# Kernel optimization log

Hardware: AMD Instinct MI355X
Metric: run time of the kernel (lower is better)

Reference implementation:

```python
import jax, jax.numpy as jnp
import numpy as np

ALPHA, GAMMA, EPS, BIG = 0.25, 2.0, 1e-7, 1e7
STRIDES = (8, 16, 32, 64, 128)
SHRINK = 0.2


def _project(boxes, fw, fh, stride):
    # shrink box around its center by SHRINK, project to feature grid (floor/ceil), clip
    cx = (boxes[..., 0] + boxes[..., 2]) * 0.5
    cy = (boxes[..., 1] + boxes[..., 3]) * 0.5
    hw = (boxes[..., 2] - boxes[..., 0]) * 0.5 * SHRINK
    hh = (boxes[..., 3] - boxes[..., 1]) * 0.5 * SHRINK
    x1 = jnp.clip(jnp.floor((cx - hw) / stride).astype(jnp.int32), 0, fw - 1)
    y1 = jnp.clip(jnp.floor((cy - hh) / stride).astype(jnp.int32), 0, fh - 1)
    x2 = jnp.clip(jnp.ceil((cx + hw) / stride).astype(jnp.int32), 1, fw)
    y2 = jnp.clip(jnp.ceil((cy + hh) / stride).astype(jnp.int32), 1, fh)
    return x1, y1, x2, y2


def _level_loss(cls_l, regr_l, boxes, labels, stride, fh, fw):
    # cls_l [B,fh,fw,C], regr_l [B,fh,fw,4], boxes [B,G,4], labels [B,G] -> loss [B,G]
    B, G = labels.shape
    x1, y1, x2, y2 = _project(boxes, fw, fh, stride)
    xs = jnp.arange(fw, dtype=jnp.int32)
    ys = jnp.arange(fh, dtype=jnp.int32)
    mx = (xs[None, None] >= x1[..., None]) & (xs[None, None] < x2[..., None])  # [B,G,fw]
    my = (ys[None, None] >= y1[..., None]) & (ys[None, None] < y2[..., None])  # [B,G,fh]
    mask = my[..., :, None] & mx[..., None, :]                                 # [B,G,fh,fw]
    denom = jnp.maximum(jnp.sum(mask, axis=(2, 3)).astype(cls_l.dtype), 1.0)   # = #positives

    # focal over one-hot(gt_label): sum_c = f0 - neg[gt] + pos[gt]
    p = jnp.clip(cls_l, EPS, 1.0 - EPS)
    neg = (1.0 - ALPHA) * p ** GAMMA * (-jnp.log1p(-p))   # per-class label=0 term
    pos = ALPHA * (1.0 - p) ** GAMMA * (-jnp.log(p))      # per-class label=1 term
    f0 = jnp.sum(neg, axis=-1)                            # [B,fh,fw]
    bidx = jnp.arange(B)[:, None]
    neg_g = neg[bidx, :, :, labels]                       # [B,G,fh,fw]
    pos_g = pos[bidx, :, :, labels]                       # [B,G,fh,fw]
    focal_map = f0[:, None] - neg_g + pos_g
    loss_cls = jnp.sum(jnp.where(mask, focal_map, 0.0), axis=(2, 3)) / denom

    # iou loss on (l,t,r,b)/(4*stride) targets, mean over region
    sx = (xs.astype(cls_l.dtype) + 0.5) * stride          # [fw]
    sy = (ys.astype(cls_l.dtype) + 0.5) * stride          # [fh]
    s = 1.0 / (4.0 * stride)
    tl = jnp.maximum(sx[None, None, None] - boxes[..., 0, None, None], 0.0) * s    # [B,G,1,fw]
    tt = jnp.maximum(sy[None, None, :, None] - boxes[..., 1, None, None], 0.0) * s  # [B,G,fh,1]
    tr = jnp.maximum(boxes[..., 2, None, None] - sx[None, None, None], 0.0) * s     # [B,G,1,fw]
    tb = jnp.maximum(boxes[..., 3, None, None] - sy[None, None, :, None], 0.0) * s  # [B,G,fh,1]
    pl = regr_l[..., 0][:, None]   # [B,1,fh,fw]
    pt = regr_l[..., 1][:, None]
    pr = regr_l[..., 2][:, None]
    pb = regr_l[..., 3][:, None]
    t_area = (tl + tr) * (tt + tb)                        # [B,G,fh,fw]
    p_area = (pl + pr) * (pt + pb)                        # [B,1,fh,fw]
    w_i = jnp.minimum(pl, tl) + jnp.minimum(pr, tr)
    h_i = jnp.minimum(pb, tb) + jnp.minimum(pt, tt)
    a_i = w_i * h_i
    a_u = t_area + p_area - a_i
    iou_map = -jnp.log((a_i + EPS) / (a_u + EPS))
    loss_iou = jnp.sum(jnp.where(mask, iou_map, 0.0), axis=(2, 3)) / denom

    empty = (x1 == x2) | (y1 == y2)                       # tf.cond 'do_not_match' branch
    return jnp.where(empty, BIG, loss_cls + loss_iou)


def _all_level_losses(cls_pred, regr_pred, gt_boxes, feature_shapes):
    fs = np.asarray(feature_shapes)
    B, C = cls_pred.shape[0], cls_pred.shape[-1]
    labels = jnp.clip(gt_boxes[..., 4].astype(jnp.int32), 0, C - 1)
    boxes = gt_boxes[..., :4]
    losses, start = [], 0
    for i, stride in enumerate(STRIDES):
        fh, fw = int(fs[i, 0]), int(fs[i, 1])
        cls_l = cls_pred[:, start:start + fh * fw].reshape(B, fh, fw, C)
        regr_l = regr_pred[:, start:start + fh * fw].reshape(B, fh, fw, 4)
        losses.append(_level_loss(cls_l, regr_l, boxes, labels, float(stride), fh, fw))
        start += fh * fw
    return jnp.stack(losses, axis=-1)   # [B,G,L]


def setup_inputs():
    key = jax.random.key(0)
    k = jax.random.split(key, 7)
    B, G, C = 8, 64, 80
    feature_shapes = np.array([[128, 128], [64, 64], [32, 32], [16, 16], [8, 8]], dtype=np.int32)
    total = int(np.prod(feature_shapes, axis=-1).sum())   # 21824 locations (1024x1024 img)
    cls_pred = jax.random.uniform(k[0], (B, total, C), jnp.float32, 0.01, 0.99)
    regr_pred = jax.random.uniform(k[1], (B, total, 4), jnp.float32, 0.05, 2.0)
    cx = jax.random.uniform(k[2], (B, G), jnp.float32, 64.0, 960.0)
    cy = jax.random.uniform(k[3], (B, G), jnp.float32, 64.0, 960.0)
    w = jax.random.uniform(k[4], (B, G), jnp.float32, 32.0, 320.0)
    h = jax.random.uniform(k[5], (B, G), jnp.float32, 32.0, 320.0)
    x1 = jnp.clip(cx - w / 2, 0.0, 1024.0)
    y1 = jnp.clip(cy - h / 2, 0.0, 1024.0)
    x2 = jnp.clip(cx + w / 2, 0.0, 1024.0)
    y2 = jnp.clip(cy + h / 2, 0.0, 1024.0)
    lbl = jax.random.randint(k[6], (B, G), 0, C).astype(jnp.float32)
    gt_boxes = jnp.stack([x1, y1, x2, y2, lbl], axis=-1)
    keep = (jnp.arange(G) < G - 16).astype(jnp.float32)   # last 16 rows are zero padding
    gt_boxes = gt_boxes * keep[None, :, None]
    return {"cls_pred": cls_pred, "regr_pred": regr_pred,
            "feature_shapes": feature_shapes, "gt_boxes": gt_boxes}


def reference(cls_pred, regr_pred, feature_shapes, gt_boxes):
    losses = _all_level_losses(cls_pred, regr_pred, gt_boxes, feature_shapes)   # [B,G,L]
    levels = jnp.argmin(losses, axis=-1).astype(jnp.int32)                      # [B,G]
    valid = jnp.sum(jnp.abs(gt_boxes[..., :4]), axis=-1) > 0                    # trim_padding_boxes
    levels = jnp.where(valid, levels, -1)                                       # padded boxes -> -1
    return levels.reshape(-1)
```

## Files before the change

### kernel.cpp

```cpp
#include <hip/hip_runtime.h>
#include <math.h>

static constexpr int B = 8;
static constexpr int G = 64;
static constexpr int C = 80;
static constexpr int TOTAL = 21824;
static constexpr float EPSF = 1e-7f;
static constexpr float BIGF = 1e7f;

__device__ __forceinline__ double wave_sum_d(double v) {
#pragma unroll
    for (int off = 32; off > 0; off >>= 1)
        v += __shfl_xor(v, off, 64);
    return v;
}

__device__ __forceinline__ float neg_fast(float x) {
    float p = fminf(fmaxf(x, EPSF), 1.0f - EPSF);
    float nl = -__logf(1.0f - p);
    return 0.75f * p * p * nl;
}

__global__ __launch_bounds__(320) void select_kernel(
        const float* __restrict__ cls, const float* __restrict__ regr,
        const float* __restrict__ gt, int* __restrict__ out) {
    const int   fws[5]     = {128, 64, 32, 16, 8};
    const int   offs[5]    = {0, 16384, 20480, 21504, 21760};
    const float strides[5] = {8.f, 16.f, 32.f, 64.f, 128.f};

    __shared__ float lloss[5];
    const int boxid = (int)blockIdx.x;
    const int l     = (int)(threadIdx.x >> 6);
    const int lane  = (int)(threadIdx.x & 63);

    const float* box = gt + (size_t)boxid * 5;
    float b0 = box[0], b1 = box[1], b2 = box[2], b3 = box[3];
    if (fabsf(b0) + fabsf(b1) + fabsf(b2) + fabsf(b3) <= 0.0f) {
        if (threadIdx.x == 0) out[boxid] = -1;
        return;
    }
    int label = (int)box[4];
    label = min(max(label, 0), C - 1);
    int b = boxid / G;

    float cx = (b0 + b2) * 0.5f, cy = (b1 + b3) * 0.5f;
    float hw = (b2 - b0) * 0.5f * 0.2f, hh = (b3 - b1) * 0.5f * 0.2f;

    const float st = strides[l];
    const int fw = fws[l];
    int x1 = min(max((int)floorf((cx - hw) / st), 0), fw - 1);
    int y1 = min(max((int)floorf((cy - hh) / st), 0), fw - 1);
    int x2 = min(max((int)ceilf((cx + hw) / st), 1), fw);
    int y2 = min(max((int)ceilf((cy + hh) / st), 1), fw);

    float loss;
    if (x1 == x2 || y1 == y2) {
        loss = BIGF;
    } else {
        int rw = x2 - x1;
        int area = rw * (y2 - y1);
        double sf = 0.0, si = 0.0;
        float s = 1.0f / (4.0f * st);
        for (int idx = lane; idx < area; idx += 64) {
            int yy = y1 + idx / rw;
            int xx = x1 + idx % rw;
            int loc = offs[l] + yy * fw + xx;
            size_t base = (size_t)b * TOTAL + (size_t)loc;

            const float4* crow = (const float4*)(cls + base * C);
            double f0d = 0.0;
#pragma unroll
            for (int i = 0; i < 20; ++i) {
                float4 v = crow[i];
                f0d += (double)neg_fast(v.x);
                f0d += (double)neg_fast(v.y);
                f0d += (double)neg_fast(v.z);
                f0d += (double)neg_fast(v.w);
            }
            float f0v = (float)f0d;

            float pv = cls[base * C + label];
            float p = fminf(fmaxf(pv, EPSF), 1.0f - EPSF);
            float neg_g = 0.75f * p * p * (-log1pf(-p));
            float omp = 1.0f - p;
            float pos_g = 0.25f * omp * omp * (-logf(p));
            sf += (double)((f0v - neg_g) + pos_g);

            const float4 r = *(const float4*)(regr + base * 4);
            float sx = ((float)xx + 0.5f) * st;
            float sy = ((float)yy + 0.5f) * st;
            float tl = fmaxf(sx - b0, 0.0f) * s;
            float tt = fmaxf(sy - b1, 0.0f) * s;
            float tr = fmaxf(b2 - sx, 0.0f) * s;
            float tb = fmaxf(b3 - sy, 0.0f) * s;
            float t_area = (tl + tr) * (tt + tb);
            float p_area = (r.x + r.z) * (r.y + r.w);
            float w_i = fminf(r.x, tl) + fminf(r.z, tr);
            float h_i = fminf(r.w, tb) + fminf(r.y, tt);
            float a_i = w_i * h_i;
            float a_u = (t_area + p_area) - a_i;
            si += (double)(-logf((a_i + EPSF) / (a_u + EPSF)));
        }
        sf = wave_sum_d(sf);
        si = wave_sum_d(si);
        float denom = (float)area;
        loss = (float)sf / denom + (float)si / denom;
    }
    if (lane == 0) lloss[l] = loss;
    __syncthreads();

    if (threadIdx.x == 0) {
        float best = lloss[0];
        int bestl = 0;
#pragma unroll
        for (int k = 1; k < 5; ++k) {
            float v = lloss[k];
            if (v < best) { best = v; bestl = k; }
        }
        out[boxid] = bestl;
    }
}

extern "C" void kernel_launch(void* const* d_in, const int* in_sizes, int n_in,
                              void* d_out, int out_size, void* d_ws, size_t ws_size,
                              hipStream_t stream) {
    const float* cls  = (const float*)d_in[0];
    const float* regr = (const float*)d_in[1];
    const float* gt   = (const float*)d_in[3];

    select_kernel<<<dim3(B * G), dim3(320), 0, stream>>>(cls, regr, gt,
                                                         (int*)d_out);
}
```

Measured before the change: 101.2 us.

## Spread class-row reduction across all waves to balance per-level work

Before, each pyramid level was handled by its own wave, so the wave for the finest level did most of the 80-class negative-focal sums while the other waves sat idle. The kernel now computes every level's region in a first pass and stores the cell lists in shared memory. All 320 threads then split each cell's class row into five 16-float segments and write the partial sums to a shared buffer. The per-level waves read those partials and only do the label and IoU work. This adds two block barriers and about 5KB of shared memory, and it assumes the total cell count per box stays within 128.

Result: faster. 92.98 us (-8.1%).

```diff
diff --git a/kernel.cpp b/kernel.cpp
--- a/kernel.cpp
+++ b/kernel.cpp
@@ -7,6 +7,7 @@
 static constexpr int TOTAL = 21824;
 static constexpr float EPSF = 1e-7f;
 static constexpr float BIGF = 1e7f;
+static constexpr int MAXC = 128;
 
 __device__ __forceinline__ double wave_sum_d(double v) {
 #pragma unroll
@@ -24,59 +25,99 @@
 __global__ __launch_bounds__(320) void select_kernel(
         const float* __restrict__ cls, const float* __restrict__ regr,
         const float* __restrict__ gt, int* __restrict__ out) {
-    const int   fws[5]     = {128, 64, 32, 16, 8};
-    const int   offs[5]    = {0, 16384, 20480, 21504, 21760};
-    const float strides[5] = {8.f, 16.f, 32.f, 64.f, 128.f};
+    const int OFFS[5] = {0, 16384, 20480, 21504, 21760};
 
+    __shared__ double part[MAXC * 5];
     __shared__ float lloss[5];
+    __shared__ int lx1[5], ly1[5], lrw[5], larea[5], lbase[6], loffl[5];
+
     const int boxid = (int)blockIdx.x;
-    const int l     = (int)(threadIdx.x >> 6);
-    const int lane  = (int)(threadIdx.x & 63);
+    const int tid   = (int)threadIdx.x;
 
     const float* box = gt + (size_t)boxid * 5;
     float b0 = box[0], b1 = box[1], b2 = box[2], b3 = box[3];
     if (fabsf(b0) + fabsf(b1) + fabsf(b2) + fabsf(b3) <= 0.0f) {
-        if (threadIdx.x == 0) out[boxid] = -1;
+        if (tid == 0) out[boxid] = -1;
         return;
     }
     int label = (int)box[4];
     label = min(max(label, 0), C - 1);
-    int b = boxid / G;
+    const int b = boxid / G;
 
     float cx = (b0 + b2) * 0.5f, cy = (b1 + b3) * 0.5f;
     float hw = (b2 - b0) * 0.5f * 0.2f, hh = (b3 - b1) * 0.5f * 0.2f;
 
-    const float st = strides[l];
-    const int fw = fws[l];
-    int x1 = min(max((int)floorf((cx - hw) / st), 0), fw - 1);
-    int y1 = min(max((int)floorf((cy - hh) / st), 0), fw - 1);
-    int x2 = min(max((int)ceilf((cx + hw) / st), 1), fw);
-    int y2 = min(max((int)ceilf((cy + hh) / st), 1), fw);
+    int ncells = 0;
+#pragma unroll
+    for (int k = 0; k < 5; ++k) {
+        const float st = (float)(8 << k);
+        const int fw = 128 >> k;
+        int x1 = min(max((int)floorf((cx - hw) / st), 0), fw - 1);
+        int y1 = min(max((int)floorf((cy - hh) / st), 0), fw - 1);
+        int x2 = min(max((int)ceilf((cx + hw) / st), 1), fw);
+        int y2 = min(max((int)ceilf((cy + hh) / st), 1), fw);
+        int rw = x2 - x1;
+        int area = ((x1 == x2) || (y1 == y2)) ? 0 : rw * (y2 - y1);
+        if (tid == 0) {
+            lx1[k] = x1; ly1[k] = y1; lrw[k] = rw;
+            larea[k] = area; lbase[k] = ncells; loffl[k] = OFFS[k];
+        }
+        ncells += area;
+    }
+    if (tid == 0) lbase[5] = ncells;
+    __syncthreads();
+
+    const int ntasks = ncells * 5;
+    for (int t = tid; t < ntasks; t += 320) {
+        int c = t / 5, seg = t - c * 5;
+        int l = 4;
+#pragma unroll
+        for (int k = 3; k >= 0; --k)
+            if (c < lbase[k + 1]) l = k;
+        int idx = c - lbase[l];
+        int rw = lrw[l];
+        int qy = idx / rw;
+        int yy = ly1[l] + qy;
+        int xx = lx1[l] + (idx - qy * rw);
+        int loc = loffl[l] + yy * (128 >> l) + xx;
+        size_t base = (size_t)b * TOTAL + (size_t)loc;
+        const float4* crow = (const float4*)(cls + base * C) + seg * 4;
+        double p = 0.0;
+#pragma unroll
+        for (int i = 0; i < 4; ++i) {
+            float4 v = crow[i];
+            p += (double)neg_fast(v.x);
+            p += (double)neg_fast(v.y);
+            p += (double)neg_fast(v.z);
+            p += (double)neg_fast(v.w);
+        }
+        part[c * 5 + seg] = p;
+    }
+    __syncthreads();
+
+    const int l    = tid >> 6;
+    const int lane = tid & 63;
+    const int area = larea[l];
 
     float loss;
-    if (x1 == x2 || y1 == y2) {
+    if (area == 0) {
         loss = BIGF;
     } else {
-        int rw = x2 - x1;
-        int area = rw * (y2 - y1);
+        const float st = (float)(8 << l);
+        const int fw = 128 >> l;
+        const int x1 = lx1[l], y1 = ly1[l], rw = lrw[l], cbase = lbase[l];
         double sf = 0.0, si = 0.0;
         float s = 1.0f / (4.0f * st);
         for (int idx = lane; idx < area; idx += 64) {
-            int yy = y1 + idx / rw;
-            int xx = x1 + idx % rw;
-            int loc = offs[l] + yy * fw + xx;
+            int qy = idx / rw;
+            int yy = y1 + qy;
+            int xx = x1 + (idx - qy * rw);
+            int loc = loffl[l] + yy * fw + xx;
             size_t base = (size_t)b * TOTAL + (size_t)loc;
+            int c = cbase + idx;
 
-            const float4* crow = (const float4*)(cls + base * C);
-            double f0d = 0.0;
-#pragma unroll
-            for (int i = 0; i < 20; ++i) {
-                float4 v = crow[i];
-                f0d += (double)neg_fast(v.x);
-                f0d += (double)neg_fast(v.y);
-                f0d += (double)neg_fast(v.z);
-                f0d += (double)neg_fast(v.w);
-            }
+            double f0d = part[c * 5] + part[c * 5 + 1] + part[c * 5 + 2] +
+                         part[c * 5 + 3] + part[c * 5 + 4];
             float f0v = (float)f0d;
 
             float pv = cls[base * C + label];
@@ -109,7 +150,7 @@
     if (lane == 0) lloss[l] = loss;
     __syncthreads();
 
-    if (threadIdx.x == 0) {
+    if (tid == 0) {
         float best = lloss[0];
         int bestl = 0;
 #pragma unroll
```
